# Performance work log

Measured on AMD Instinct MI355X. Metric: run time of the kernel, lower is better.

Reference implementation:

```python
import jax, jax.numpy as jnp
import numpy as np

B, S, D = 32, 4096, 512   # batch, seq_len, input_dim
A, K = 3, 4               # attractor_dim, num_attractors
OUT = 512                 # output_dim


def setup_inputs() -> dict:
    key = jax.random.key(0)
    ks = jax.random.split(key, 10)
    s = 0.02
    return {
        "x": jax.random.normal(ks[0], (B, S, D), dtype=jnp.float32),
        "centers": jax.random.normal(ks[1], (K, A), dtype=jnp.float32),
        "Wa": jax.random.normal(ks[2], (D, A), dtype=jnp.float32) * s,
        "ba": jnp.zeros((A,), dtype=jnp.float32),
        "Wh": jax.random.normal(ks[3], (A, 2 * A), dtype=jnp.float32) * 0.5,
        "bh": jnp.zeros((2 * A,), dtype=jnp.float32),
        "Wk": jax.random.normal(ks[4], (2 * A, K), dtype=jnp.float32) * 0.5,
        "bk": jnp.zeros((K,), dtype=jnp.float32),
        "Wout": jax.random.normal(ks[5], (K * D, OUT), dtype=jnp.float32) * s,
        "bout": jnp.zeros((OUT,), dtype=jnp.float32),
    }


def reference(x, centers, Wa, ba, Wh, bh, Wk, bk, Wout, bout):
    # project to attractor space: [B,S,A]
    af = jnp.einsum("bsd,da->bsa", x, Wa) + ba
    # L2 distance to each attractor center: [B,S,K]
    diff = af[:, :, :, None] - centers.T[None, None, :, :]   # [B,S,A,K]
    distances = jnp.sqrt(jnp.sum(diff * diff, axis=2))
    # tiny MLP weights (batched over all timesteps at once): [B,S,K]
    base = jax.nn.relu(af @ Wh + bh) @ Wk + bk
    distance_weights = jax.nn.softmax(-distances, axis=-1)
    final_weights = jax.nn.softmax(base + distance_weights, axis=-1)
    # attractor-weighted pooling over time, concatenated attractor-major: [B, K*D]
    pooled = jnp.einsum("bsk,bsd->bkd", final_weights, x).reshape(x.shape[0], -1)
    return pooled @ Wout + bout
```

## Files before the change

kernel.cpp:

```cpp
#include <hip/hip_runtime.h>
#include <cstdint>
#include <cstddef>

#define BB 32
#define SS 4096
#define DD 512
#define AA 3
#define KK 4
#define OUTD 512

#define TR 16
#define XROW 520

__device__ __forceinline__ void load_tile(const float* __restrict__ xb,
                                          int s0, int tid, float4 st[8]) {
    #pragma unroll
    for (int t = 0; t < 8; ++t) {
        const int idx = tid + t * 256;
        const int row = idx >> 7;
        const int c4  = (idx & 127) << 2;
        st[t] = *(const float4*)(xb + (size_t)(s0 + row) * DD + c4);
    }
}

__global__ __launch_bounds__(256) void fused_pool_kernel(
    const float* __restrict__ x, const float* __restrict__ centers,
    const float* __restrict__ Wa, const float* __restrict__ ba,
    const float* __restrict__ Wh, const float* __restrict__ bh,
    const float* __restrict__ Wk, const float* __restrict__ bk,
    float* __restrict__ partial)
{
    __shared__ alignas(16) float  xs[TR * XROW];
    __shared__ alignas(16) float  wat[AA * DD];
    __shared__ float  sw[68];
    __shared__ float4 fw_sh[TR];

    const int tid   = threadIdx.x;
    const int b     = blockIdx.y;
    const int chunk = blockIdx.x;
    const int nch   = gridDim.x;
    const int rows_per_block = SS / nch;
    const int nit   = rows_per_block / TR;

    if (tid < 12)      sw[tid] = centers[tid];
    else if (tid < 15) sw[tid] = ba[tid - 12];
    else if (tid < 33) sw[tid] = Wh[tid - 15];
    else if (tid < 39) sw[tid] = bh[tid - 33];
    else if (tid < 63) sw[tid] = Wk[tid - 39];
    else if (tid < 67) sw[tid] = bk[tid - 63];
    for (int d = tid; d < DD; d += 256) {
        wat[0 * DD + d] = Wa[d * 3 + 0];
        wat[1 * DD + d] = Wa[d * 3 + 1];
        wat[2 * DD + d] = Wa[d * 3 + 2];
    }

    const int g   = tid >> 4;
    const int l16 = tid & 15;
    const int c2  = tid * 2;
    const int s_base = chunk * rows_per_block;
    const float* xb = x + (size_t)b * SS * DD;

    float2 acc[KK];
    #pragma unroll
    for (int k = 0; k < KK; ++k) { acc[k].x = 0.f; acc[k].y = 0.f; }

    float4 st[8];
    load_tile(xb, s_base, tid, st);

    #pragma unroll 1
    for (int it = 0; it < nit; ++it) {
        __syncthreads();
        #pragma unroll
        for (int t = 0; t < 8; ++t) {
            const int idx = tid + t * 256;
            *(float4*)(xs + (idx >> 7) * XROW + ((idx & 127) << 2)) = st[t];
        }
        if (it + 1 < nit)
            load_tile(xb, s_base + (it + 1) * TR, tid, st);
        __syncthreads();

        {
            const float* xrow = xs + g * XROW;
            float p0 = 0.f, p1 = 0.f, p2 = 0.f;
            #pragma unroll
            for (int i = 0; i < 8; ++i) {
                const int c = l16 * 4 + i * 64;
                float4 v  = *(const float4*)(xrow + c);
                float4 w0 = *(const float4*)(wat + c);
                float4 w1 = *(const float4*)(wat + DD + c);
                float4 w2 = *(const float4*)(wat + 2 * DD + c);
                p0 += v.x * w0.x + v.y * w0.y + v.z * w0.z + v.w * w0.w;
                p1 += v.x * w1.x + v.y * w1.y + v.z * w1.z + v.w * w1.w;
                p2 += v.x * w2.x + v.y * w2.y + v.z * w2.z + v.w * w2.w;
            }
            #pragma unroll
            for (int off = 8; off >= 1; off >>= 1) {
                p0 += __shfl_xor(p0, off);
                p1 += __shfl_xor(p1, off);
                p2 += __shfl_xor(p2, off);
            }
            const float af0 = p0 + sw[12];
            const float af1 = p1 + sw[13];
            const float af2 = p2 + sw[14];

            float dist[KK];
            #pragma unroll
            for (int k = 0; k < KK; ++k) {
                float da = af0 - sw[k * 3 + 0];
                float db = af1 - sw[k * 3 + 1];
                float dc = af2 - sw[k * 3 + 2];
                dist[k] = sqrtf(da * da + db * db + dc * dc);
            }
            float mn = fminf(fminf(dist[0], dist[1]), fminf(dist[2], dist[3]));
            float e[KK]; float esum = 0.f;
            #pragma unroll
            for (int k = 0; k < KK; ++k) { e[k] = __expf(mn - dist[k]); esum += e[k]; }
            const float einv = 1.0f / esum;

            float h[6];
            #pragma unroll
            for (int i6 = 0; i6 < 6; ++i6) {
                float v = af0 * sw[15 + i6] + af1 * sw[21 + i6]
                        + af2 * sw[27 + i6] + sw[33 + i6];
                h[i6] = fmaxf(v, 0.0f);
            }
            float logit[KK];
            #pragma unroll
            for (int k = 0; k < KK; ++k) {
                float v = sw[63 + k];
                #pragma unroll
                for (int i6 = 0; i6 < 6; ++i6) v += h[i6] * sw[39 + i6 * 4 + k];
                logit[k] = v + e[k] * einv;
            }
            float mx = fmaxf(fmaxf(logit[0], logit[1]), fmaxf(logit[2], logit[3]));
            float f0 = __expf(logit[0] - mx), f1 = __expf(logit[1] - mx);
            float f2 = __expf(logit[2] - mx), f3 = __expf(logit[3] - mx);
            const float finv = 1.0f / (f0 + f1 + f2 + f3);
            if (l16 == 0)
                fw_sh[g] = make_float4(f0 * finv, f1 * finv, f2 * finv, f3 * finv);
        }
        __syncthreads();

        #pragma unroll
        for (int r = 0; r < TR; ++r) {
            float2 xv = *(const float2*)(xs + r * XROW + c2);
            float4 f  = fw_sh[r];
            acc[0].x += f.x * xv.x; acc[0].y += f.x * xv.y;
            acc[1].x += f.y * xv.x; acc[1].y += f.y * xv.y;
            acc[2].x += f.z * xv.x; acc[2].y += f.z * xv.y;
            acc[3].x += f.w * xv.x; acc[3].y += f.w * xv.y;
        }
    }

    float* pp = partial + ((size_t)b * nch + chunk) * (KK * DD);
    #pragma unroll
    for (int k = 0; k < KK; ++k)
        *(float2*)(pp + k * DD + c2) = acc[k];
}

__global__ __launch_bounds__(256) void out_gemm_kernel(
    const float* __restrict__ partial, const float* __restrict__ Wout,
    const float* __restrict__ bout, float* __restrict__ out, int nch)
{
    __shared__ float  p_sh[2048];
    __shared__ float4 red4[4][64];
    const int tid = threadIdx.x;
    const int cc = blockIdx.x, b = blockIdx.y;

    for (int j = tid; j < 2048; j += 256) {
        const float* pj = partial + (size_t)b * nch * 2048 + j;
        float s = 0.f;
        for (int c = 0; c < nch; ++c) s += pj[(size_t)c * 2048];
        p_sh[j] = s;
    }
    __syncthreads();

    const int q  = tid & 63;
    const int js = tid >> 6;
    const int colbase = cc * 256 + q * 4;
    const float* wp = Wout + (size_t)(js * 512) * OUTD + colbase;
    float4 a = make_float4(0.f, 0.f, 0.f, 0.f);
    #pragma unroll 8
    for (int j = 0; j < 512; ++j) {
        float4 w = *(const float4*)(wp + (size_t)j * OUTD);
        float  p = p_sh[js * 512 + j];
        a.x += p * w.x; a.y += p * w.y; a.z += p * w.z; a.w += p * w.w;
    }
    red4[js][q] = a;
    __syncthreads();

    const int qq = tid >> 2, e = tid & 3;
    float s = 0.f;
    #pragma unroll
    for (int s4 = 0; s4 < 4; ++s4)
        s += ((const float*)&red4[s4][qq])[e];
    out[b * OUTD + cc * 256 + tid] = s + bout[cc * 256 + tid];
}

extern "C" void kernel_launch(void* const* d_in, const int* in_sizes, int n_in,
                              void* d_out, int out_size, void* d_ws, size_t ws_size,
                              hipStream_t stream) {
    (void)in_sizes; (void)n_in; (void)out_size;
    const float* x       = (const float*)d_in[0];
    const float* centers = (const float*)d_in[1];
    const float* Wa      = (const float*)d_in[2];
    const float* ba      = (const float*)d_in[3];
    const float* Wh      = (const float*)d_in[4];
    const float* bh      = (const float*)d_in[5];
    const float* Wk      = (const float*)d_in[6];
    const float* bk      = (const float*)d_in[7];
    const float* Wout    = (const float*)d_in[8];
    const float* bout    = (const float*)d_in[9];
    float* out     = (float*)d_out;
    float* partial = (float*)d_ws;

    int nch = 32;
    while (nch > 1 && (size_t)BB * nch * 2048 * sizeof(float) > ws_size) nch >>= 1;

    fused_pool_kernel<<<dim3(nch, BB), 256, 0, stream>>>(
        x, centers, Wa, ba, Wh, bh, Wk, bk, partial);
    out_gemm_kernel<<<dim3(2, BB), 256, 0, stream>>>(partial, Wout, bout, out, nch);
}
```

Measured before the change: 516.0 us.

## Pool from register tiles with double-buffered prefetch and widen output GEMM grid

The pooling accumulation now reads x straight from each thread's prefetched registers (float4 per thread, split across two row halves) instead of re-reading the shared tile. The loop is unrolled by two with ping-pong register buffers, which removes one barrier per iteration. The halves are reduced through shared memory at the end. The chunk count becomes a compile-time constant, dropping the workspace-size check, and the output GEMM launches 4 column blocks with an 8-way split and float4 partial reduction. This raises register pressure and assumes the workspace is large enough.

```diff
diff --git a/kernel.cpp b/kernel.cpp
--- a/kernel.cpp
+++ b/kernel.cpp
@@ -9,7 +9,10 @@
 #define KK 4
 #define OUTD 512
 
+#define NCH 32
+#define ROWS_PER_BLOCK (SS / NCH)
 #define TR 16
+#define NIT (ROWS_PER_BLOCK / TR)
 #define XROW 520
 
 __device__ __forceinline__ void load_tile(const float* __restrict__ xb,
@@ -38,9 +41,6 @@
     const int tid   = threadIdx.x;
     const int b     = blockIdx.y;
     const int chunk = blockIdx.x;
-    const int nch   = gridDim.x;
-    const int rows_per_block = SS / nch;
-    const int nit   = rows_per_block / TR;
 
     if (tid < 12)      sw[tid] = centers[tid];
     else if (tid < 15) sw[tid] = ba[tid - 12];
@@ -54,29 +54,24 @@
         wat[2 * DD + d] = Wa[d * 3 + 2];
     }
 
-    const int g   = tid >> 4;
-    const int l16 = tid & 15;
-    const int c2  = tid * 2;
-    const int s_base = chunk * rows_per_block;
+    const int g    = tid >> 4;
+    const int l16  = tid & 15;
+    const int half = tid >> 7;
+    const int c4   = (tid & 127) << 2;
+    const int s_base = chunk * ROWS_PER_BLOCK;
     const float* xb = x + (size_t)b * SS * DD;
 
-    float2 acc[KK];
-    #pragma unroll
-    for (int k = 0; k < KK; ++k) { acc[k].x = 0.f; acc[k].y = 0.f; }
-
-    float4 st[8];
-    load_tile(xb, s_base, tid, st);
-
-    #pragma unroll 1
-    for (int it = 0; it < nit; ++it) {
-        __syncthreads();
-        #pragma unroll
-        for (int t = 0; t < 8; ++t) {
-            const int idx = tid + t * 256;
-            *(float4*)(xs + (idx >> 7) * XROW + ((idx & 127) << 2)) = st[t];
-        }
-        if (it + 1 < nit)
-            load_tile(xb, s_base + (it + 1) * TR, tid, st);
+    float4 acc0 = {0,0,0,0}, acc1 = {0,0,0,0}, acc2 = {0,0,0,0}, acc3 = {0,0,0,0};
+
+    float4 stA[8], stB[8];
+    load_tile(xb, s_base, tid, stA);
+
+    auto step = [&](float4 (&cur)[8], float4 (&nxt)[8], int it) {
+        #pragma unroll
+        for (int t = 0; t < 8; ++t)
+            *(float4*)(xs + (half + 2 * t) * XROW + c4) = cur[t];
+        if (it + 1 < NIT)
+            load_tile(xb, s_base + (it + 1) * TR, tid, nxt);
         __syncthreads();
 
         {
@@ -142,65 +137,100 @@
         __syncthreads();
 
         #pragma unroll
-        for (int r = 0; r < TR; ++r) {
-            float2 xv = *(const float2*)(xs + r * XROW + c2);
-            float4 f  = fw_sh[r];
-            acc[0].x += f.x * xv.x; acc[0].y += f.x * xv.y;
-            acc[1].x += f.y * xv.x; acc[1].y += f.y * xv.y;
-            acc[2].x += f.z * xv.x; acc[2].y += f.z * xv.y;
-            acc[3].x += f.w * xv.x; acc[3].y += f.w * xv.y;
+        for (int t = 0; t < 8; ++t) {
+            float4 v = cur[t];
+            float4 f = fw_sh[half + 2 * t];
+            acc0.x += f.x * v.x; acc0.y += f.x * v.y; acc0.z += f.x * v.z; acc0.w += f.x * v.w;
+            acc1.x += f.y * v.x; acc1.y += f.y * v.y; acc1.z += f.y * v.z; acc1.w += f.y * v.w;
+            acc2.x += f.z * v.x; acc2.y += f.z * v.y; acc2.z += f.z * v.z; acc2.w += f.z * v.w;
+            acc3.x += f.w * v.x; acc3.y += f.w * v.y; acc3.z += f.w * v.z; acc3.w += f.w * v.w;
         }
-    }
-
-    float* pp = partial + ((size_t)b * nch + chunk) * (KK * DD);
-    #pragma unroll
-    for (int k = 0; k < KK; ++k)
-        *(float2*)(pp + k * DD + c2) = acc[k];
+    };
+
+    #pragma unroll 1
+    for (int it = 0; it < NIT; it += 2) {
+        step(stA, stB, it);
+        step(stB, stA, it + 1);
+    }
+
+    __syncthreads();
+    float4* red = (float4*)xs;
+    if (half == 1) {
+        red[(tid - 128) * 4 + 0] = acc0;
+        red[(tid - 128) * 4 + 1] = acc1;
+        red[(tid - 128) * 4 + 2] = acc2;
+        red[(tid - 128) * 4 + 3] = acc3;
+    }
+    __syncthreads();
+    if (half == 0) {
+        float4 o0 = red[tid * 4 + 0], o1 = red[tid * 4 + 1];
+        float4 o2 = red[tid * 4 + 2], o3 = red[tid * 4 + 3];
+        acc0.x += o0.x; acc0.y += o0.y; acc0.z += o0.z; acc0.w += o0.w;
+        acc1.x += o1.x; acc1.y += o1.y; acc1.z += o1.z; acc1.w += o1.w;
+        acc2.x += o2.x; acc2.y += o2.y; acc2.z += o2.z; acc2.w += o2.w;
+        acc3.x += o3.x; acc3.y += o3.y; acc3.z += o3.z; acc3.w += o3.w;
+        float* pp = partial + ((size_t)b * NCH + chunk) * (KK * DD);
+        *(float4*)(pp + 0 * DD + c4) = acc0;
+        *(float4*)(pp + 1 * DD + c4) = acc1;
+        *(float4*)(pp + 2 * DD + c4) = acc2;
+        *(float4*)(pp + 3 * DD + c4) = acc3;
+    }
 }
 
 __global__ __launch_bounds__(256) void out_gemm_kernel(
     const float* __restrict__ partial, const float* __restrict__ Wout,
-    const float* __restrict__ bout, float* __restrict__ out, int nch)
+    const float* __restrict__ bout, float* __restrict__ out)
 {
     __shared__ float  p_sh[2048];
-    __shared__ float4 red4[4][64];
+    __shared__ float4 red4[8][32];
     const int tid = threadIdx.x;
     const int cc = blockIdx.x, b = blockIdx.y;
 
-    for (int j = tid; j < 2048; j += 256) {
-        const float* pj = partial + (size_t)b * nch * 2048 + j;
+    {
+        const float4* pbase = (const float4*)(partial + (size_t)b * NCH * 2048);
+        #pragma unroll
+        for (int s = 0; s < 2; ++s) {
+            const int slot = tid + s * 256;
+            float4 a = {0,0,0,0};
+            #pragma unroll 4
+            for (int c = 0; c < NCH; ++c) {
+                float4 v = pbase[(size_t)c * 512 + slot];
+                a.x += v.x; a.y += v.y; a.z += v.z; a.w += v.w;
+            }
+            *(float4*)(p_sh + slot * 4) = a;
+        }
+    }
+    __syncthreads();
+
+    const int q  = tid & 31;
+    const int js = tid >> 5;
+    const int colbase = cc * 128 + q * 4;
+    const float* wp = Wout + (size_t)(js * 256) * OUTD + colbase;
+    float4 a = {0,0,0,0};
+    #pragma unroll 8
+    for (int j = 0; j < 256; ++j) {
+        float4 w = *(const float4*)(wp + (size_t)j * OUTD);
+        float  p = p_sh[js * 256 + j];
+        a.x += p * w.x; a.y += p * w.y; a.z += p * w.z; a.w += p * w.w;
+    }
+    red4[js][q] = a;
+    __syncthreads();
+
+    if (tid < 128) {
+        const int qq = tid >> 2, e = tid & 3;
         float s = 0.f;
-        for (int c = 0; c < nch; ++c) s += pj[(size_t)c * 2048];
-        p_sh[j] = s;
-    }
-    __syncthreads();
-
-    const int q  = tid & 63;
-    const int js = tid >> 6;
-    const int colbase = cc * 256 + q * 4;
-    const float* wp = Wout + (size_t)(js * 512) * OUTD + colbase;
-    float4 a = make_float4(0.f, 0.f, 0.f, 0.f);
-    #pragma unroll 8
-    for (int j = 0; j < 512; ++j) {
-        float4 w = *(const float4*)(wp + (size_t)j * OUTD);
-        float  p = p_sh[js * 512 + j];
-        a.x += p * w.x; a.y += p * w.y; a.z += p * w.z; a.w += p * w.w;
-    }
-    red4[js][q] = a;
-    __syncthreads();
-
-    const int qq = tid >> 2, e = tid & 3;
-    float s = 0.f;
-    #pragma unroll
-    for (int s4 = 0; s4 < 4; ++s4)
-        s += ((const float*)&red4[s4][qq])[e];
-    out[b * OUTD + cc * 256 + tid] = s + bout[cc * 256 + tid];
+        #pragma unroll
+        for (int s8 = 0; s8 < 8; ++s8)
+            s += ((const float*)&red4[s8][qq])[e];
+        const int col = cc * 128 + tid;
+        out[b * OUTD + col] = s + bout[col];
+    }
 }
 
 extern "C" void kernel_launch(void* const* d_in, const int* in_sizes, int n_in,
                               void* d_out, int out_size, void* d_ws, size_t ws_size,
                               hipStream_t stream) {
-    (void)in_sizes; (void)n_in; (void)out_size;
+    (void)in_sizes; (void)n_in; (void)out_size; (void)ws_size;
     const float* x       = (const float*)d_in[0];
     const float* centers = (const float*)d_in[1];
     const float* Wa      = (const float*)d_in[2];
@@ -214,10 +244,7 @@
     float* out     = (float*)d_out;
     float* partial = (float*)d_ws;
 
-    int nch = 32;
-    while (nch > 1 && (size_t)BB * nch * 2048 * sizeof(float) > ws_size) nch >>= 1;
-
-    fused_pool_kernel<<<dim3(nch, BB), 256, 0, stream>>>(
+    fused_pool_kernel<<<dim3(NCH, BB), 256, 0, stream>>>(
         x, centers, Wa, ba, Wh, bh, Wk, bk, partial);
-    out_gemm_kernel<<<dim3(2, BB), 256, 0, stream>>>(partial, Wout, bout, out, nch);
-}
+    out_gemm_kernel<<<dim3(4, BB), 256, 0, stream>>>(partial, Wout, bout, out);
+}
```

New measurement: 413.6 us. -19.8%, faster.
